# Performance work log

Measured on AMD Instinct MI355X. Metric: run time of the kernel, lower is better.

Reference implementation:

```python
import jax, jax.numpy as jnp
import numpy as np

NP_, NL_ = 2048, 128          # protein / ligand node counts
D_IN, D_OUT, NUM_HEAD = 128, 128, 1
NEG_SLOPE, EPS = 0.2, 1e-10


def setup_inputs() -> dict:
    key = jax.random.key(0)
    k1, k2, k3, k4 = jax.random.split(key, 4)
    node_feat_protein = jax.random.normal(k1, (NP_, D_IN), jnp.float32)
    node_feat_ligand = jax.random.normal(k2, (NL_, D_IN), jnp.float32)
    W = jax.random.normal(k3, (D_IN, D_OUT), jnp.float32) / np.sqrt(D_IN)
    b = jnp.zeros((D_OUT,), jnp.float32)
    query = jax.random.normal(k4, (NUM_HEAD, 2 * D_OUT // NUM_HEAD), jnp.float32) * 0.1
    # full bipartite cross-graph edges, both directions (as in get_graph_intra)
    ip = jnp.repeat(jnp.arange(NP_, dtype=jnp.int32), NL_)          # [Np*Nl]
    il = jnp.tile(jnp.arange(NL_, dtype=jnp.int32) + NP_, NP_)      # [Np*Nl]
    node_in = jnp.concatenate([ip, il])
    node_out = jnp.concatenate([il, ip])
    edge_list = jnp.stack([node_in, node_out], axis=1)              # [2*Np*Nl, 2]
    return {"node_feat_protein": node_feat_protein,
            "node_feat_ligand": node_feat_ligand,
            "edge_list": edge_list,
            "W": W, "b": b, "query": query}


def _gat_forward(node_feat, edge_list, W, b, query):
    N = node_feat.shape[0]
    H = query.shape[0]
    # add self-loops (torchdrug GraphAttentionConv.message)
    self_idx = jnp.arange(N, dtype=edge_list.dtype)
    node_in = jnp.concatenate([edge_list[:, 0], self_idx])
    node_out = jnp.concatenate([edge_list[:, 1], self_idx])
    E = node_in.shape[0]

    hidden = node_feat @ W + b                                  # [N, D_OUT]
    h_in = hidden[node_in]                                      # [E, D_OUT]
    h_out = hidden[node_out]                                    # [E, D_OUT]
    # key = [h_in ; h_out] split into heads
    key_eh = jnp.concatenate([h_in, h_out], axis=-1).reshape(E, H, -1)
    logits = jnp.einsum("hd,ehd->eh", query, key_eh)            # [E, H]
    logits = jax.nn.leaky_relu(logits, NEG_SLOPE)
    # segment softmax over destination nodes (every node has a self-loop)
    seg_max = jax.ops.segment_max(logits, node_out, num_segments=N)
    att = jnp.exp(logits - seg_max[node_out])                   # edge_weight == 1
    seg_sum = jax.ops.segment_sum(att, node_out, num_segments=N)
    att = att / (seg_sum[node_out] + EPS)                       # [E, H]

    value = h_in.reshape(E, H, -1)                              # [E, H, D/H]
    message = (att[..., None] * value).reshape(E, -1)           # [E, D_OUT]
    update = jax.ops.segment_sum(message, node_out, num_segments=N)
    return jax.nn.relu(update)                                  # default activation


def reference(node_feat_protein, node_feat_ligand, edge_list, W, b, query):
    node_feat = jnp.concatenate([node_feat_protein, node_feat_ligand])
    out = _gat_forward(node_feat, edge_list, W, b, query)
    n_p = node_feat_protein.shape[0]
    return out[:n_p], out[n_p:]
```

## Files before the change

### kernel.cpp

```cpp
#include <hip/hip_runtime.h>
#include <math.h>


#define NP 2048
#define NL 128
#define NN 2176

static __device__ float g_hidden[NN * 128];
static __device__ float g_ain[NN];
static __device__ float g_aout[NN];
static __device__ float g_part[16 * NL * 128];
static __device__ float g_einvL[NL];

__device__ __forceinline__ float lrelu(float x) { return x > 0.f ? x : 0.2f * x; }

__global__ __launch_bounds__(256) void k1_hidden(
    const float* xp, const float* xl, const float* W,
    const float* b, const float* q)
{
    __shared__ float Xs[8][128];
    const int tid = threadIdx.x;
    const int cg = tid & 31;
    const int rs = tid >> 5;
    const int base = blockIdx.x * 8;
    {
        int flat = tid * 4, row = flat >> 7, col = flat & 127;
        int n = base + row;
        const float* src = (n < NP) ? xp + n * 128 : xl + (n - NP) * 128;
        *(float4*)&Xs[row][col] = *(const float4*)(src + col);
    }
    __syncthreads();

    float4 a = *(const float4*)(b + cg * 4);
    #pragma unroll 8
    for (int k = 0; k < 128; ++k) {
        float4 w4 = *(const float4*)(W + k * 128 + cg * 4);
        float x = Xs[rs][k];
        a.x = fmaf(x, w4.x, a.x); a.y = fmaf(x, w4.y, a.y);
        a.z = fmaf(x, w4.z, a.z); a.w = fmaf(x, w4.w, a.w);
    }
    *(float4*)(g_hidden + (base + rs) * 128 + cg * 4) = a;

    float4 q1v = *(const float4*)(q + cg * 4);
    float4 q2v = *(const float4*)(q + 128 + cg * 4);
    float p1 = q1v.x*a.x + q1v.y*a.y + q1v.z*a.z + q1v.w*a.w;
    float p2 = q2v.x*a.x + q2v.y*a.y + q2v.z*a.z + q2v.w*a.w;
    #pragma unroll
    for (int off = 16; off; off >>= 1) {
        p1 += __shfl_xor(p1, off);
        p2 += __shfl_xor(p2, off);
    }
    if (cg == 0) { g_ain[base + rs] = p1; g_aout[base + rs] = p2; }
}

__global__ __launch_bounds__(256) void k2_attn(float* out)
{
    __shared__ __align__(16) float Ws[8][128];
    __shared__ float cself[8];
    __shared__ float As[NP];
    __shared__ __align__(16) float ws2[16 * 128];
    __shared__ float sm[16], sinv[16];

    const int tid = threadIdx.x;
    const int bid = blockIdx.x;

    if (bid < 256) {
        const int cg = tid & 31, rs = tid >> 5;
        const int p = bid * 8 + rs;
        const float ao = g_aout[p];
        const float sl = lrelu(g_ain[p] + ao);

        float lg0 = lrelu(g_ain[NP + cg] + ao);
        float lg1 = lrelu(g_ain[NP + 32 + cg] + ao);
        float lg2 = lrelu(g_ain[NP + 64 + cg] + ao);
        float lg3 = lrelu(g_ain[NP + 96 + cg] + ao);
        float m = fmaxf(fmaxf(lg0, lg1), fmaxf(lg2, lg3));
        #pragma unroll
        for (int off = 16; off; off >>= 1) m = fmaxf(m, __shfl_xor(m, off));
        m = fmaxf(m, sl);
        float e0 = expf(lg0 - m), e1 = expf(lg1 - m);
        float e2 = expf(lg2 - m), e3 = expf(lg3 - m);
        float s = e0 + e1 + e2 + e3;
        #pragma unroll
        for (int off = 16; off; off >>= 1) s += __shfl_xor(s, off);
        const float es = expf(sl - m);
        const float inv = 1.f / (s + es + 1e-10f);
        Ws[rs][cg]      = e0 * inv;
        Ws[rs][cg + 32] = e1 * inv;
        Ws[rs][cg + 64] = e2 * inv;
        Ws[rs][cg + 96] = e3 * inv;
        if (cg == 0) cself[rs] = es * inv;
        __syncthreads();

        float4 h = *(const float4*)(g_hidden + p * 128 + cg * 4);
        float c0 = cself[rs];
        float4 acc;
        acc.x = c0 * h.x; acc.y = c0 * h.y; acc.z = c0 * h.z; acc.w = c0 * h.w;
        #pragma unroll 8
        for (int l = 0; l < 128; ++l) {
            float4 h4 = *(const float4*)(g_hidden + (NP + l) * 128 + cg * 4);
            float x = Ws[rs][l];
            acc.x = fmaf(x, h4.x, acc.x); acc.y = fmaf(x, h4.y, acc.y);
            acc.z = fmaf(x, h4.z, acc.z); acc.w = fmaf(x, h4.w, acc.w);
        }
        acc.x = acc.x > 0.f ? acc.x : 0.f;
        acc.y = acc.y > 0.f ? acc.y : 0.f;
        acc.z = acc.z > 0.f ? acc.z : 0.f;
        acc.w = acc.w > 0.f ? acc.w : 0.f;
        *(float4*)(out + p * 128 + cg * 4) = acc;
    } else {
        const int lb = bid - 256;
        const int pchunk = lb >> 3, lgroup = lb & 7;
        const int p0 = pchunk * 128, lbase = lgroup * 16;

        for (int t = tid; t < 512; t += 256)
            *(float4*)&As[t * 4] = *(const float4*)(g_ain + t * 4);
        __syncthreads();

        const int li = tid >> 4, tt = tid & 15;
        const int l = lbase + li;
        const float ao = g_aout[NP + l];
        float mx = -1e30f;
        for (int p = tt; p < NP; p += 16)
            mx = fmaxf(mx, lrelu(As[p] + ao));
        #pragma unroll
        for (int off = 8; off; off >>= 1) mx = fmaxf(mx, __shfl_xor(mx, off));
        const float sl = lrelu(g_ain[NP + l] + ao);
        const float m = fmaxf(mx, sl);
        float s = 0.f;
        for (int p = tt; p < NP; p += 16)
            s += expf(lrelu(As[p] + ao) - m);
        #pragma unroll
        for (int off = 8; off; off >>= 1) s += __shfl_xor(s, off);
        const float es = expf(sl - m);
        const float inv = 1.f / (s + es + 1e-10f);
        if (tt == 0) {
            sm[li] = m; sinv[li] = inv;
            if (pchunk == 0) g_einvL[l] = es * inv;
        }
        __syncthreads();

        for (int t = tid; t < 2048; t += 256) {
            int li2 = t >> 7, pi = t & 127;
            float ao2 = g_aout[NP + lbase + li2];
            ws2[t] = expf(lrelu(As[p0 + pi] + ao2) - sm[li2]) * sinv[li2];
        }
        __syncthreads();

        const int cc = tid & 127, lh = tid >> 7;
        float acc[8];
        #pragma unroll
        for (int u = 0; u < 8; ++u) acc[u] = 0.f;
        for (int pi = 0; pi < 128; pi += 4) {
            float h0 = g_hidden[(p0 + pi) * 128 + cc];
            float h1 = g_hidden[(p0 + pi + 1) * 128 + cc];
            float h2 = g_hidden[(p0 + pi + 2) * 128 + cc];
            float h3 = g_hidden[(p0 + pi + 3) * 128 + cc];
            #pragma unroll
            for (int u = 0; u < 8; ++u) {
                float4 w4 = *(float4*)&ws2[(lh * 8 + u) * 128 + pi];
                acc[u] = fmaf(w4.w, h3, fmaf(w4.z, h2,
                         fmaf(w4.y, h1, fmaf(w4.x, h0, acc[u]))));
            }
        }
        #pragma unroll
        for (int u = 0; u < 8; ++u)
            g_part[(pchunk * 128 + lbase + lh * 8 + u) * 128 + cc] = acc[u];
    }
}

__global__ __launch_bounds__(256) void k3_finish(float* out)
{
    const int idx = blockIdx.x * 256 + threadIdx.x;
    const int l = idx >> 7, c = idx & 127;
    float s = g_einvL[l] * g_hidden[(NP + l) * 128 + c];
    #pragma unroll
    for (int k = 0; k < 16; ++k)
        s += g_part[(k * 128 + l) * 128 + c];
    out[(NP + l) * 128 + c] = s > 0.f ? s : 0.f;
}

extern "C" void kernel_launch(void* const* d_in, const int* in_sizes, int n_in,
                              void* d_out, int out_size, void* d_ws, size_t ws_size,
                              hipStream_t stream) {
    const float* xp = (const float*)d_in[0];
    const float* xl = (const float*)d_in[1];
    const float* W  = (const float*)d_in[3];
    const float* b  = (const float*)d_in[4];
    const float* q  = (const float*)d_in[5];
    float* out = (float*)d_out;

    k1_hidden<<<272, 256, 0, stream>>>(xp, xl, W, b, q);
    k2_attn<<<384, 256, 0, stream>>>(out);
    k3_finish<<<64, 256, 0, stream>>>(out);
}
```

Measured before the change: 103.8 us.

## Double grid sizes and batch global loads to raise memory-level parallelism

k1 now uses 128-thread blocks with 4 rows each, doubling the block count. The protein-side attention in k2 maps each 64-lane wave to one protein row with float2 columns, so there are twice as many blocks. Loops in k1, k2 and k3 now issue batches of 16 or 8 global loads into registers before the FMAs, so more loads are in flight at once. The goal is to hide load latency in these small, latency-bound kernels, at the cost of more register pressure and narrower per-thread vector loads.

```diff
diff --git a/kernel.cpp b/kernel.cpp
--- a/kernel.cpp
+++ b/kernel.cpp
@@ -14,15 +14,15 @@
 
 __device__ __forceinline__ float lrelu(float x) { return x > 0.f ? x : 0.2f * x; }
 
-__global__ __launch_bounds__(256) void k1_hidden(
+__global__ __launch_bounds__(128) void k1_hidden(
     const float* xp, const float* xl, const float* W,
     const float* b, const float* q)
 {
-    __shared__ float Xs[8][128];
+    __shared__ float Xs[4][128];
     const int tid = threadIdx.x;
     const int cg = tid & 31;
     const int rs = tid >> 5;
-    const int base = blockIdx.x * 8;
+    const int base = blockIdx.x * 4;
     {
         int flat = tid * 4, row = flat >> 7, col = flat & 127;
         int n = base + row;
@@ -32,12 +32,17 @@
     __syncthreads();
 
     float4 a = *(const float4*)(b + cg * 4);
-    #pragma unroll 8
-    for (int k = 0; k < 128; ++k) {
-        float4 w4 = *(const float4*)(W + k * 128 + cg * 4);
-        float x = Xs[rs][k];
-        a.x = fmaf(x, w4.x, a.x); a.y = fmaf(x, w4.y, a.y);
-        a.z = fmaf(x, w4.z, a.z); a.w = fmaf(x, w4.w, a.w);
+    for (int kk = 0; kk < 128; kk += 16) {
+        float4 wb[16];
+        #pragma unroll
+        for (int i = 0; i < 16; ++i)
+            wb[i] = *(const float4*)(W + (kk + i) * 128 + cg * 4);
+        #pragma unroll
+        for (int i = 0; i < 16; ++i) {
+            float x = Xs[rs][kk + i];
+            a.x = fmaf(x, wb[i].x, a.x); a.y = fmaf(x, wb[i].y, a.y);
+            a.z = fmaf(x, wb[i].z, a.z); a.w = fmaf(x, wb[i].w, a.w);
+        }
     }
     *(float4*)(g_hidden + (base + rs) * 128 + cg * 4) = a;
 
@@ -55,8 +60,8 @@
 
 __global__ __launch_bounds__(256) void k2_attn(float* out)
 {
-    __shared__ __align__(16) float Ws[8][128];
-    __shared__ float cself[8];
+    __shared__ __align__(16) float Ws[4][128];
+    __shared__ float cself[4];
     __shared__ float As[NP];
     __shared__ __align__(16) float ws2[16 * 128];
     __shared__ float sm[16], sinv[16];
@@ -64,52 +69,51 @@
     const int tid = threadIdx.x;
     const int bid = blockIdx.x;
 
-    if (bid < 256) {
-        const int cg = tid & 31, rs = tid >> 5;
-        const int p = bid * 8 + rs;
+    if (bid < 512) {
+        const int rs = tid >> 6, lane = tid & 63;
+        const int p = bid * 4 + rs;
         const float ao = g_aout[p];
         const float sl = lrelu(g_ain[p] + ao);
 
-        float lg0 = lrelu(g_ain[NP + cg] + ao);
-        float lg1 = lrelu(g_ain[NP + 32 + cg] + ao);
-        float lg2 = lrelu(g_ain[NP + 64 + cg] + ao);
-        float lg3 = lrelu(g_ain[NP + 96 + cg] + ao);
-        float m = fmaxf(fmaxf(lg0, lg1), fmaxf(lg2, lg3));
-        #pragma unroll
-        for (int off = 16; off; off >>= 1) m = fmaxf(m, __shfl_xor(m, off));
+        float lg0 = lrelu(g_ain[NP + lane] + ao);
+        float lg1 = lrelu(g_ain[NP + 64 + lane] + ao);
+        float m = fmaxf(lg0, lg1);
+        #pragma unroll
+        for (int off = 32; off; off >>= 1) m = fmaxf(m, __shfl_xor(m, off));
         m = fmaxf(m, sl);
         float e0 = expf(lg0 - m), e1 = expf(lg1 - m);
-        float e2 = expf(lg2 - m), e3 = expf(lg3 - m);
-        float s = e0 + e1 + e2 + e3;
-        #pragma unroll
-        for (int off = 16; off; off >>= 1) s += __shfl_xor(s, off);
+        float s = e0 + e1;
+        #pragma unroll
+        for (int off = 32; off; off >>= 1) s += __shfl_xor(s, off);
         const float es = expf(sl - m);
         const float inv = 1.f / (s + es + 1e-10f);
-        Ws[rs][cg]      = e0 * inv;
-        Ws[rs][cg + 32] = e1 * inv;
-        Ws[rs][cg + 64] = e2 * inv;
-        Ws[rs][cg + 96] = e3 * inv;
-        if (cg == 0) cself[rs] = es * inv;
-        __syncthreads();
-
-        float4 h = *(const float4*)(g_hidden + p * 128 + cg * 4);
+        Ws[rs][lane]      = e0 * inv;
+        Ws[rs][lane + 64] = e1 * inv;
+        if (lane == 0) cself[rs] = es * inv;
+        __syncthreads();
+
+        const int c2 = lane * 2;
+        float2 h = *(const float2*)(g_hidden + p * 128 + c2);
         float c0 = cself[rs];
-        float4 acc;
-        acc.x = c0 * h.x; acc.y = c0 * h.y; acc.z = c0 * h.z; acc.w = c0 * h.w;
-        #pragma unroll 8
-        for (int l = 0; l < 128; ++l) {
-            float4 h4 = *(const float4*)(g_hidden + (NP + l) * 128 + cg * 4);
-            float x = Ws[rs][l];
-            acc.x = fmaf(x, h4.x, acc.x); acc.y = fmaf(x, h4.y, acc.y);
-            acc.z = fmaf(x, h4.z, acc.z); acc.w = fmaf(x, h4.w, acc.w);
-        }
-        acc.x = acc.x > 0.f ? acc.x : 0.f;
-        acc.y = acc.y > 0.f ? acc.y : 0.f;
-        acc.z = acc.z > 0.f ? acc.z : 0.f;
-        acc.w = acc.w > 0.f ? acc.w : 0.f;
-        *(float4*)(out + p * 128 + cg * 4) = acc;
+        float ax = c0 * h.x, ay = c0 * h.y;
+        for (int kk = 0; kk < 128; kk += 16) {
+            float2 hb[16];
+            #pragma unroll
+            for (int i = 0; i < 16; ++i)
+                hb[i] = *(const float2*)(g_hidden + (NP + kk + i) * 128 + c2);
+            #pragma unroll
+            for (int i = 0; i < 16; ++i) {
+                float x = Ws[rs][kk + i];
+                ax = fmaf(x, hb[i].x, ax);
+                ay = fmaf(x, hb[i].y, ay);
+            }
+        }
+        float2 o;
+        o.x = ax > 0.f ? ax : 0.f;
+        o.y = ay > 0.f ? ay : 0.f;
+        *(float2*)(out + p * 128 + c2) = o;
     } else {
-        const int lb = bid - 256;
+        const int lb = bid - 512;
         const int pchunk = lb >> 3, lgroup = lb & 7;
         const int p0 = pchunk * 128, lbase = lgroup * 16;
 
@@ -151,16 +155,18 @@
         float acc[8];
         #pragma unroll
         for (int u = 0; u < 8; ++u) acc[u] = 0.f;
-        for (int pi = 0; pi < 128; pi += 4) {
-            float h0 = g_hidden[(p0 + pi) * 128 + cc];
-            float h1 = g_hidden[(p0 + pi + 1) * 128 + cc];
-            float h2 = g_hidden[(p0 + pi + 2) * 128 + cc];
-            float h3 = g_hidden[(p0 + pi + 3) * 128 + cc];
+        for (int pi = 0; pi < 128; pi += 8) {
+            float hb[8];
+            #pragma unroll
+            for (int i = 0; i < 8; ++i)
+                hb[i] = g_hidden[(p0 + pi + i) * 128 + cc];
             #pragma unroll
             for (int u = 0; u < 8; ++u) {
-                float4 w4 = *(float4*)&ws2[(lh * 8 + u) * 128 + pi];
-                acc[u] = fmaf(w4.w, h3, fmaf(w4.z, h2,
-                         fmaf(w4.y, h1, fmaf(w4.x, h0, acc[u]))));
+                float a0 = acc[u];
+                #pragma unroll
+                for (int i = 0; i < 8; ++i)
+                    a0 = fmaf(ws2[(lh * 8 + u) * 128 + pi + i], hb[i], a0);
+                acc[u] = a0;
             }
         }
         #pragma unroll
@@ -173,10 +179,13 @@
 {
     const int idx = blockIdx.x * 256 + threadIdx.x;
     const int l = idx >> 7, c = idx & 127;
+    float v[16];
+    #pragma unroll
+    for (int k = 0; k < 16; ++k)
+        v[k] = g_part[(k * 128 + l) * 128 + c];
     float s = g_einvL[l] * g_hidden[(NP + l) * 128 + c];
     #pragma unroll
-    for (int k = 0; k < 16; ++k)
-        s += g_part[(k * 128 + l) * 128 + c];
+    for (int k = 0; k < 16; ++k) s += v[k];
     out[(NP + l) * 128 + c] = s > 0.f ? s : 0.f;
 }
 
@@ -190,7 +199,7 @@
     const float* q  = (const float*)d_in[5];
     float* out = (float*)d_out;
 
-    k1_hidden<<<272, 256, 0, stream>>>(xp, xl, W, b, q);
-    k2_attn<<<384, 256, 0, stream>>>(out);
+    k1_hidden<<<544, 128, 0, stream>>>(xp, xl, W, b, q);
+    k2_attn<<<640, 256, 0, stream>>>(out);
     k3_finish<<<64, 256, 0, stream>>>(out);
 }
```

New measurement: 102.8 us. No clear change (-1.0%).
